# Kernel optimization log

Hardware: AMD Instinct MI355X
Metric: run time of the kernel (lower is better)

## Reference

```python
import jax, jax.numpy as jnp
import numpy as np

N_NODES = 100000
N_EDGES = 1600000
IN_CH, MID_CH, BOT_CH = 128, 128, 64


def setup_inputs() -> dict:
    key = jax.random.key(0)
    ks = jax.random.split(key, 10)
    x = jax.random.normal(ks[0], (N_NODES, IN_CH), dtype=jnp.float32)
    edge_index = jax.random.randint(ks[1], (2, N_EDGES), 0, N_NODES, dtype=jnp.int64)
    s = 0.05
    # GCNConv weights follow torch Linear convention: out = x @ W.T + b (bias added post-aggregation)
    W1 = jax.random.normal(ks[2], (MID_CH, IN_CH), dtype=jnp.float32) * s
    b1 = jnp.zeros((MID_CH,), dtype=jnp.float32)
    W2 = jax.random.normal(ks[3], (BOT_CH, MID_CH), dtype=jnp.float32) * s
    b2 = jnp.zeros((BOT_CH,), dtype=jnp.float32)
    W3 = jax.random.normal(ks[4], (MID_CH, BOT_CH), dtype=jnp.float32) * s
    b3 = jnp.zeros((MID_CH,), dtype=jnp.float32)
    W4 = jax.random.normal(ks[5], (IN_CH, MID_CH), dtype=jnp.float32) * s
    b4 = jnp.zeros((IN_CH,), dtype=jnp.float32)
    return {"x": x, "edge_index": edge_index,
            "W1": W1, "b1": b1, "W2": W2, "b2": b2,
            "W3": W3, "b3": b3, "W4": W4, "b4": b4}


def _gcn_conv(x, src, dst, norm, W, b, n):
    # linear transform first (small GEMM), then gather-normalize-scatter
    h = x @ W.T                                   # [N, out]
    msg = h[src] * norm[:, None]                  # [E+N, out] gathered messages
    out = jax.ops.segment_sum(msg, dst, num_segments=n)
    return out + b


def reference(x, edge_index, W1, b1, W2, b2, W3, b3, W4, b4):
    n = N_NODES
    # add self-loops (PyG GCNConv default)
    loop = jnp.arange(n, dtype=edge_index.dtype)
    src = jnp.concatenate([edge_index[0], loop])
    dst = jnp.concatenate([edge_index[1], loop])
    # symmetric degree normalization: deg includes self-loops -> deg >= 1
    deg = jax.ops.segment_sum(jnp.ones_like(dst, dtype=x.dtype), dst, num_segments=n)
    dinv = jax.lax.rsqrt(deg)
    norm = dinv[src] * dinv[dst]                  # [E+N]
    # encoder
    h = jax.nn.relu(_gcn_conv(x, src, dst, norm, W1, b1, n))
    z = _gcn_conv(h, src, dst, norm, W2, b2, n)
    # decoder
    h = jax.nn.relu(_gcn_conv(z, src, dst, norm, W3, b3, n))
    out = _gcn_conv(h, src, dst, norm, W4, b4, n)
    return out
```

## Files before the change

### kernel.cpp

```cpp
#include <hip/hip_runtime.h>

typedef unsigned int u32;
typedef unsigned short u16;
typedef short bf16x4 __attribute__((ext_vector_type(4)));
typedef short bf16x8 __attribute__((ext_vector_type(8)));
typedef float f32x4 __attribute__((ext_vector_type(4)));
typedef int i32x4 __attribute__((ext_vector_type(4)));
typedef long long i64x2 __attribute__((ext_vector_type(2)));

__device__ inline u16 f2bf_rne(float f) {
    u32 b = __float_as_uint(f);
    return (u16)((b + 0x7FFFu + ((b >> 16) & 1u)) >> 16);
}
__device__ inline u32 packbf2(float lo, float hi) {
    return (u32)f2bf_rne(lo) | ((u32)f2bf_rne(hi) << 16);
}
__device__ inline float bf2f(u16 h) { return __uint_as_float((u32)h << 16); }
__device__ inline float2 bfpair(u32 q) {
    float2 f;
    f.x = __uint_as_float(q << 16);
    f.y = __uint_as_float(q & 0xFFFF0000u);
    return f;
}

__global__ void k_detect(const int* __restrict__ p, int n_int32, u32* __restrict__ flag) {
    __shared__ int s[256];
    int tid = threadIdx.x;
    int acc = 0;
    int limit = n_int32 < 2048 ? n_int32 : 2048;
    for (int i = 1 + 2 * tid; i < limit; i += 512) acc |= p[i];
    s[tid] = acc;
    __syncthreads();
    for (int o = 128; o > 0; o >>= 1) {
        if (tid < o) s[tid] |= s[tid + o];
        __syncthreads();
    }
    if (tid == 0) *flag = (s[0] == 0) ? 1u : 0u;
}

template <int CIN, int COUT>
__global__ void k_wpack(const float* __restrict__ W, u16* __restrict__ Wpk) {
    int i = blockIdx.x * 256 + threadIdx.x;
    if (i >= CIN * COUT) return;
    int o = i / CIN, k = i % CIN;
    int fi = o >> 4, l15 = o & 15;
    int ks = k >> 5, w = k & 31;
    int h = w >> 4, l4 = (w & 15) >> 2, off = w & 3;
    int lane = l4 * 16 + l15;
    int e = h * 4 + off;
    constexpr int KS = CIN / 32;
    Wpk[(size_t)(((fi * KS + ks) * 64 + lane) * 8 + e)] = f2bf_rne(W[i]);
}

__global__ void k_init(u32* __restrict__ cnt, int N) {
    int i = blockIdx.x * blockDim.x + threadIdx.x;
    if (i < N) cnt[i] = 0u;
}

__global__ __launch_bounds__(256) void k_filld(const void* __restrict__ ei,
                                               const u32* __restrict__ flag,
                                               u32* __restrict__ cnt,
                                               int* __restrict__ col, int E, int N) {
    int grp = blockIdx.x & 7;
    int sub = blockIdx.x >> 3;
    int nsub = gridDim.x >> 3;
    int lo = (int)((long long)N * grp >> 3);
    int hi = (int)((long long)N * (grp + 1) >> 3);

    if (*flag) {
        const long long* p = (const long long*)ei;
        const i64x2* d2 = (const i64x2*)(p + E);
        int E2 = E >> 1;
        for (int i = sub * 256 + threadIdx.x; i < E2; i += nsub * 256) {
            i64x2 d = __builtin_nontemporal_load(d2 + i);
            int e = i << 1;
            int dx = (int)d.x, dy = (int)d.y;
            if (dx >= lo && dx < hi) {
                u32 slot = atomicAdd(&cnt[dx], 1u);
                if (slot < 64u) col[(size_t)dx * 64 + slot] =
                    (int)__builtin_nontemporal_load(p + e);
            }
            if (dy >= lo && dy < hi) {
                u32 slot = atomicAdd(&cnt[dy], 1u);
                if (slot < 64u) col[(size_t)dy * 64 + slot] =
                    (int)__builtin_nontemporal_load(p + e + 1);
            }
        }
        for (int e = (E2 << 1) + sub * 256 + threadIdx.x; e < E; e += nsub * 256) {
            int d = (int)__builtin_nontemporal_load(p + E + e);
            if (d >= lo && d < hi) {
                u32 slot = atomicAdd(&cnt[d], 1u);
                if (slot < 64u) col[(size_t)d * 64 + slot] =
                    (int)__builtin_nontemporal_load(p + e);
            }
        }
    } else {
        const int* p = (const int*)ei;
        const i32x4* d4 = (const i32x4*)(p + E);
        int E4 = E >> 2;
        for (int i = sub * 256 + threadIdx.x; i < E4; i += nsub * 256) {
            i32x4 d = __builtin_nontemporal_load(d4 + i);
            int e = i << 2;
            if (d.x >= lo && d.x < hi) {
                u32 slot = atomicAdd(&cnt[d.x], 1u);
                if (slot < 64u) col[(size_t)d.x * 64 + slot] =
                    __builtin_nontemporal_load(p + e);
            }
            if (d.y >= lo && d.y < hi) {
                u32 slot = atomicAdd(&cnt[d.y], 1u);
                if (slot < 64u) col[(size_t)d.y * 64 + slot] =
                    __builtin_nontemporal_load(p + e + 1);
            }
            if (d.z >= lo && d.z < hi) {
                u32 slot = atomicAdd(&cnt[d.z], 1u);
                if (slot < 64u) col[(size_t)d.z * 64 + slot] =
                    __builtin_nontemporal_load(p + e + 2);
            }
            if (d.w >= lo && d.w < hi) {
                u32 slot = atomicAdd(&cnt[d.w], 1u);
                if (slot < 64u) col[(size_t)d.w * 64 + slot] =
                    __builtin_nontemporal_load(p + e + 3);
            }
        }
        for (int e = (E4 << 2) + sub * 256 + threadIdx.x; e < E; e += nsub * 256) {
            int d = __builtin_nontemporal_load(p + E + e);
            if (d >= lo && d < hi) {
                u32 slot = atomicAdd(&cnt[d], 1u);
                if (slot < 64u) col[(size_t)d * 64 + slot] =
                    __builtin_nontemporal_load(p + e);
            }
        }
    }
}

__global__ void k_dinv(const u32* __restrict__ cnt, float* __restrict__ dinv, int N) {
    int i = blockIdx.x * blockDim.x + threadIdx.x;
    if (i < N) dinv[i] = rsqrtf((float)(cnt[i] + 1u));
}

template <int CIN, int COUT, int MODE, bool IN_F32>
__global__ __launch_bounds__(512, 4) void k_mgemm(const void* __restrict__ Xv,
                                                  const u16* __restrict__ Wpk,
                                                  const float* __restrict__ aux,
                                                  u16* __restrict__ Gout, int N,
                                                  int tiles, int tpb) {
    constexpr int PITCH = CIN + 8;
    constexpr int EPITCH = COUT + 8;
    constexpr int KS = CIN / 32;
    constexpr int NT = COUT / 32;
    constexpr int CHUNKS = COUT / 8;
    __shared__ __align__(16) u16 sX[64 * PITCH];
    __shared__ __align__(16) u16 sE[64 * EPITCH];

    int tid = threadIdx.x, wid = tid >> 6, lane = tid & 63;
    int l15 = lane & 15, l4 = lane >> 4;
    int rg = wid >> 1;
    int cg = wid & 1;

    bf16x8 wfrag[NT][KS];
#pragma unroll
    for (int nt = 0; nt < NT; ++nt) {
        int fi = cg * NT + nt;
#pragma unroll
        for (int ks = 0; ks < KS; ++ks)
            wfrag[nt][ks] = *(const bf16x8*)&Wpk[(size_t)(((fi * KS + ks) * 64 + lane) * 8)];
    }
    float bv[NT];
    if (MODE == 1) {
#pragma unroll
        for (int nt = 0; nt < NT; ++nt) bv[nt] = aux[cg * (COUT / 2) + nt * 16 + l15];
    }

    int t0 = blockIdx.x * tpb;
    int t1 = t0 + tpb; if (t1 > tiles) t1 = tiles;

    for (int t = t0; t < t1; ++t) {
        int rowbase = t * 64;

        if (IN_F32) {
            const float* Xf = (const float*)Xv;
            for (int i = tid * 8; i < 64 * CIN; i += 512 * 8) {
                int r = i / CIN, k = i % CIN;
                int row = rowbase + r;
                if (row >= N) row = N - 1;
                const float4* xp = (const float4*)(Xf + (size_t)row * CIN + k);
                float4 a = xp[0], b = xp[1];
                uint4 pk;
                pk.x = packbf2(a.x, a.y);
                pk.y = packbf2(a.z, a.w);
                pk.z = packbf2(b.x, b.y);
                pk.w = packbf2(b.z, b.w);
                *(uint4*)&sX[r * PITCH + k] = pk;
            }
        } else {
            const u16* Xb = (const u16*)Xv;
            for (int i = tid * 8; i < 64 * CIN; i += 512 * 8) {
                int r = i / CIN, k = i % CIN;
                int row = rowbase + r;
                if (row >= N) row = N - 1;
                *(bf16x8*)&sX[r * PITCH + k] = *(const bf16x8*)&Xb[(size_t)row * CIN + k];
            }
        }
        __syncthreads();

        f32x4 acc[NT];
#pragma unroll
        for (int nt = 0; nt < NT; ++nt) acc[nt] = (f32x4){0.f, 0.f, 0.f, 0.f};

        const u16* xrow = &sX[(rg * 16 + l15) * PITCH + 4 * l4];
#pragma unroll
        for (int ks = 0; ks < KS; ++ks) {
            bf16x4 a0 = *(const bf16x4*)(xrow + ks * 32);
            bf16x4 a1 = *(const bf16x4*)(xrow + ks * 32 + 16);
            bf16x8 av = __builtin_shufflevector(a0, a1, 0, 1, 2, 3, 4, 5, 6, 7);
#pragma unroll
            for (int nt = 0; nt < NT; ++nt)
                acc[nt] = __builtin_amdgcn_mfma_f32_16x16x32_bf16(av, wfrag[nt][ks], acc[nt], 0, 0, 0);
        }

#pragma unroll
        for (int i = 0; i < 4; ++i) {
            int rl = rg * 16 + 4 * l4 + i;
            int row = rowbase + rl;
            int rc = row < N ? row : N - 1;
            float s = (MODE == 0) ? aux[rc] : 0.f;
#pragma unroll
            for (int nt = 0; nt < NT; ++nt) {
                float a = acc[nt][i];
                float o = (MODE == 0) ? a * s : fmaxf(a + bv[nt], 0.f);
                sE[rl * EPITCH + cg * (COUT / 2) + nt * 16 + l15] = f2bf_rne(o);
            }
        }
        __syncthreads();

        for (int a = tid; a < 64 * CHUNKS; a += 512) {
            int rl = a / CHUNKS, ch = a % CHUNKS;
            int row = rowbase + rl;
            if (row < N)
                *(uint4*)&Gout[(size_t)row * COUT + ch * 8] =
                    *(const uint4*)&sE[rl * EPITCH + ch * 8];
        }
    }
}

__global__ __launch_bounds__(512, 2) void k_mgemm34(const u16* __restrict__ Xb,
                                                    const u16* __restrict__ Wp3,
                                                    const u16* __restrict__ Wp4,
                                                    const float* __restrict__ b3,
                                                    const float* __restrict__ dinv,
                                                    u16* __restrict__ Gout, int N) {
    constexpr int P1 = 72;
    constexpr int P2 = 136;
    __shared__ __align__(16) u16 sW4[128 * 128];
    __shared__ __align__(16) u16 sBuf[64 * P2];
    __shared__ __align__(16) u16 sH[64 * P2];

    int tid = threadIdx.x, wid = tid >> 6, lane = tid & 63;
    int l15 = lane & 15, l4 = lane >> 4;
    int rg = wid >> 1, cg = wid & 1;
    int rowbase = blockIdx.x * 64;

    bf16x8 wf3[4][2];
#pragma unroll
    for (int nt = 0; nt < 4; ++nt) {
        int fi = cg * 4 + nt;
#pragma unroll
        for (int ks = 0; ks < 2; ++ks)
            wf3[nt][ks] = *(const bf16x8*)&Wp3[(size_t)(((fi * 2 + ks) * 64 + lane) * 8)];
    }
    float bv[4];
#pragma unroll
    for (int nt = 0; nt < 4; ++nt) bv[nt] = b3[cg * 64 + nt * 16 + l15];

    for (int i = tid * 8; i < 128 * 128; i += 512 * 8)
        *(bf16x8*)&sW4[i] = *(const bf16x8*)&Wp4[i];

    for (int i = tid * 8; i < 64 * 64; i += 512 * 8) {
        int r = i / 64, k = i % 64;
        int row = rowbase + r;
        if (row >= N) row = N - 1;
        *(bf16x8*)&sBuf[r * P1 + k] = *(const bf16x8*)&Xb[(size_t)row * 64 + k];
    }
    __syncthreads();

    f32x4 acc[4];
#pragma unroll
    for (int nt = 0; nt < 4; ++nt) acc[nt] = (f32x4){0.f, 0.f, 0.f, 0.f};
    {
        const u16* xrow = &sBuf[(rg * 16 + l15) * P1 + 4 * l4];
#pragma unroll
        for (int ks = 0; ks < 2; ++ks) {
            bf16x4 a0 = *(const bf16x4*)(xrow + ks * 32);
            bf16x4 a1 = *(const bf16x4*)(xrow + ks * 32 + 16);
            bf16x8 av = __builtin_shufflevector(a0, a1, 0, 1, 2, 3, 4, 5, 6, 7);
#pragma unroll
            for (int nt = 0; nt < 4; ++nt)
                acc[nt] = __builtin_amdgcn_mfma_f32_16x16x32_bf16(av, wf3[nt][ks], acc[nt], 0, 0, 0);
        }
    }
#pragma unroll
    for (int i = 0; i < 4; ++i) {
        int rl = rg * 16 + 4 * l4 + i;
#pragma unroll
        for (int nt = 0; nt < 4; ++nt)
            sH[rl * P2 + cg * 64 + nt * 16 + l15] = f2bf_rne(fmaxf(acc[nt][i] + bv[nt], 0.f));
    }
    __syncthreads();

#pragma unroll
    for (int nt = 0; nt < 4; ++nt) acc[nt] = (f32x4){0.f, 0.f, 0.f, 0.f};
    {
        const u16* xrow = &sH[(rg * 16 + l15) * P2 + 4 * l4];
#pragma unroll
        for (int ks = 0; ks < 4; ++ks) {
            bf16x4 a0 = *(const bf16x4*)(xrow + ks * 32);
            bf16x4 a1 = *(const bf16x4*)(xrow + ks * 32 + 16);
            bf16x8 av = __builtin_shufflevector(a0, a1, 0, 1, 2, 3, 4, 5, 6, 7);
#pragma unroll
            for (int nt = 0; nt < 4; ++nt) {
                int fi = cg * 4 + nt;
                bf16x8 bw = *(const bf16x8*)&sW4[(size_t)(((fi * 4 + ks) * 64 + lane) * 8)];
                acc[nt] = __builtin_amdgcn_mfma_f32_16x16x32_bf16(av, bw, acc[nt], 0, 0, 0);
            }
        }
    }
#pragma unroll
    for (int i = 0; i < 4; ++i) {
        int rl = rg * 16 + 4 * l4 + i;
        int row = rowbase + rl;
        int rc = row < N ? row : N - 1;
        float s = dinv[rc];
#pragma unroll
        for (int nt = 0; nt < 4; ++nt)
            sBuf[rl * P2 + cg * 64 + nt * 16 + l15] = f2bf_rne(acc[nt][i] * s);
    }
    __syncthreads();

    for (int a = tid; a < 64 * 16; a += 512) {
        int rl = a / 16, ch = a % 16;
        int row = rowbase + rl;
        if (row < N)
            *(uint4*)&Gout[(size_t)row * 128 + ch * 8] = *(const uint4*)&sBuf[rl * P2 + ch * 8];
    }
}

template <bool OUT_BF16, bool RELU, bool HAS_BIAS>
__global__ __launch_bounds__(256) void k_spmm128(const u32* __restrict__ Gq,
                                                 const u32* __restrict__ cnt,
                                                 const int* __restrict__ col,
                                                 const float* __restrict__ dinv,
                                                 const float* __restrict__ bias,
                                                 void* __restrict__ Y, int N) {
    int wid = threadIdx.x >> 6, lane = threadIdx.x & 63;
    int v0 = blockIdx.x * 8 + wid * 2;
    if (v0 >= N) return;
    int v1 = v0 + 1;
    bool has1 = (v1 < N);

    float2 acc0 = bfpair(Gq[(size_t)v0 * 64 + lane]);
    int e0 = v0 << 6;
    int c0 = (int)cnt[v0]; if (c0 > 64) c0 = 64;
    int f0 = e0 + c0;
    float2 acc1 = {0.f, 0.f};
    int e1 = 0, f1 = 0;
    if (has1) {
        acc1 = bfpair(Gq[(size_t)v1 * 64 + lane]);
        e1 = v1 << 6;
        int c1 = (int)cnt[v1]; if (c1 > 64) c1 = 64;
        f1 = e1 + c1;
    }

    while (e0 + 8 <= f0 && e1 + 8 <= f1) {
        int u0[8], u1[8];
#pragma unroll
        for (int j = 0; j < 8; ++j) u0[j] = col[e0 + j];
#pragma unroll
        for (int j = 0; j < 8; ++j) u1[j] = col[e1 + j];
        u32 q0[8], q1[8];
#pragma unroll
        for (int j = 0; j < 8; ++j) q0[j] = Gq[(size_t)u0[j] * 64 + lane];
#pragma unroll
        for (int j = 0; j < 8; ++j) q1[j] = Gq[(size_t)u1[j] * 64 + lane];
#pragma unroll
        for (int j = 0; j < 8; ++j) {
            float2 a = bfpair(q0[j]);
            acc0.x += a.x; acc0.y += a.y;
        }
#pragma unroll
        for (int j = 0; j < 8; ++j) {
            float2 a = bfpair(q1[j]);
            acc1.x += a.x; acc1.y += a.y;
        }
        e0 += 8; e1 += 8;
    }
    for (; e0 + 8 <= f0; e0 += 8) {
        int u[8];
#pragma unroll
        for (int j = 0; j < 8; ++j) u[j] = col[e0 + j];
        u32 q[8];
#pragma unroll
        for (int j = 0; j < 8; ++j) q[j] = Gq[(size_t)u[j] * 64 + lane];
#pragma unroll
        for (int j = 0; j < 8; ++j) {
            float2 a = bfpair(q[j]);
            acc0.x += a.x; acc0.y += a.y;
        }
    }
    for (; e1 + 8 <= f1; e1 += 8) {
        int u[8];
#pragma unroll
        for (int j = 0; j < 8; ++j) u[j] = col[e1 + j];
        u32 q[8];
#pragma unroll
        for (int j = 0; j < 8; ++j) q[j] = Gq[(size_t)u[j] * 64 + lane];
#pragma unroll
        for (int j = 0; j < 8; ++j) {
            float2 a = bfpair(q[j]);
            acc1.x += a.x; acc1.y += a.y;
        }
    }
    for (; e0 < f0; ++e0) {
        float2 a = bfpair(Gq[(size_t)col[e0] * 64 + lane]);
        acc0.x += a.x; acc0.y += a.y;
    }
    for (; e1 < f1; ++e1) {
        float2 a = bfpair(Gq[(size_t)col[e1] * 64 + lane]);
        acc1.x += a.x; acc1.y += a.y;
    }

    {
        float s = dinv[v0];
        float rx = acc0.x * s, ry = acc0.y * s;
        if (HAS_BIAS) { rx += bias[2 * lane]; ry += bias[2 * lane + 1]; }
        if (RELU) { rx = fmaxf(rx, 0.f); ry = fmaxf(ry, 0.f); }
        if (OUT_BF16) ((u32*)Y)[(size_t)v0 * 64 + lane] = packbf2(rx, ry);
        else {
            float2 o2; o2.x = rx; o2.y = ry;
            *(float2*)((float*)Y + (size_t)v0 * 128 + 2 * lane) = o2;
        }
    }
    if (has1) {
        float s = dinv[v1];
        float rx = acc1.x * s, ry = acc1.y * s;
        if (HAS_BIAS) { rx += bias[2 * lane]; ry += bias[2 * lane + 1]; }
        if (RELU) { rx = fmaxf(rx, 0.f); ry = fmaxf(ry, 0.f); }
        if (OUT_BF16) ((u32*)Y)[(size_t)v1 * 64 + lane] = packbf2(rx, ry);
        else {
            float2 o2; o2.x = rx; o2.y = ry;
            *(float2*)((float*)Y + (size_t)v1 * 128 + 2 * lane) = o2;
        }
    }
}

template <bool OUT_BF16, bool RELU, bool HAS_BIAS, bool PRESCALE>
__global__ __launch_bounds__(256) void k_spmm64(const u16* __restrict__ G16,
                                                const u32* __restrict__ cnt,
                                                const int* __restrict__ col,
                                                const float* __restrict__ dinv,
                                                const float* __restrict__ bias,
                                                void* __restrict__ Y, int N) {
    int wid = threadIdx.x >> 6, lane = threadIdx.x & 63;
    int v0 = blockIdx.x * 8 + wid * 2;
    if (v0 >= N) return;
    int v1 = v0 + 1;
    bool has1 = (v1 < N);

    float acc0 = bf2f(G16[(size_t)v0 * 64 + lane]);
    int e0 = v0 << 6;
    int c0 = (int)cnt[v0]; if (c0 > 64) c0 = 64;
    int f0 = e0 + c0;
    float acc1 = 0.f;
    int e1 = 0, f1 = 0;
    if (has1) {
        acc1 = bf2f(G16[(size_t)v1 * 64 + lane]);
        e1 = v1 << 6;
        int c1 = (int)cnt[v1]; if (c1 > 64) c1 = 64;
        f1 = e1 + c1;
    }

    while (e0 + 8 <= f0 && e1 + 8 <= f1) {
        int u0[8], u1[8];
#pragma unroll
        for (int j = 0; j < 8; ++j) u0[j] = col[e0 + j];
#pragma unroll
        for (int j = 0; j < 8; ++j) u1[j] = col[e1 + j];
        u16 g0[8], g1[8];
#pragma unroll
        for (int j = 0; j < 8; ++j) g0[j] = G16[(size_t)u0[j] * 64 + lane];
#pragma unroll
        for (int j = 0; j < 8; ++j) g1[j] = G16[(size_t)u1[j] * 64 + lane];
        acc0 += ((bf2f(g0[0]) + bf2f(g0[1])) + (bf2f(g0[2]) + bf2f(g0[3]))) +
                ((bf2f(g0[4]) + bf2f(g0[5])) + (bf2f(g0[6]) + bf2f(g0[7])));
        acc1 += ((bf2f(g1[0]) + bf2f(g1[1])) + (bf2f(g1[2]) + bf2f(g1[3]))) +
                ((bf2f(g1[4]) + bf2f(g1[5])) + (bf2f(g1[6]) + bf2f(g1[7])));
        e0 += 8; e1 += 8;
    }
    for (; e0 + 8 <= f0; e0 += 8) {
        int u[8];
#pragma unroll
        for (int j = 0; j < 8; ++j) u[j] = col[e0 + j];
        u16 g[8];
#pragma unroll
        for (int j = 0; j < 8; ++j) g[j] = G16[(size_t)u[j] * 64 + lane];
        acc0 += ((bf2f(g[0]) + bf2f(g[1])) + (bf2f(g[2]) + bf2f(g[3]))) +
                ((bf2f(g[4]) + bf2f(g[5])) + (bf2f(g[6]) + bf2f(g[7])));
    }
    for (; e1 + 8 <= f1; e1 += 8) {
        int u[8];
#pragma unroll
        for (int j = 0; j < 8; ++j) u[j] = col[e1 + j];
        u16 g[8];
#pragma unroll
        for (int j = 0; j < 8; ++j) g[j] = G16[(size_t)u[j] * 64 + lane];
        acc1 += ((bf2f(g[0]) + bf2f(g[1])) + (bf2f(g[2]) + bf2f(g[3]))) +
                ((bf2f(g[4]) + bf2f(g[5])) + (bf2f(g[6]) + bf2f(g[7])));
    }
    for (; e0 < f0; ++e0) acc0 += bf2f(G16[(size_t)col[e0] * 64 + lane]);
    for (; e1 < f1; ++e1) acc1 += bf2f(G16[(size_t)col[e1] * 64 + lane]);

    {
        float s = dinv[v0];
        float r = acc0 * s;
        if (HAS_BIAS) r += bias[lane];
        if (RELU) r = fmaxf(r, 0.f);
        if (PRESCALE) r *= s;
        if (OUT_BF16) ((u16*)Y)[(size_t)v0 * 64 + lane] = f2bf_rne(r);
        else          ((float*)Y)[(size_t)v0 * 64 + lane] = r;
    }
    if (has1) {
        float s = dinv[v1];
        float r = acc1 * s;
        if (HAS_BIAS) r += bias[lane];
        if (RELU) r = fmaxf(r, 0.f);
        if (PRESCALE) r *= s;
        if (OUT_BF16) ((u16*)Y)[(size_t)v1 * 64 + lane] = f2bf_rne(r);
        else          ((float*)Y)[(size_t)v1 * 64 + lane] = r;
    }
}

extern "C" void kernel_launch(void* const* d_in, const int* in_sizes, int n_in,
                              void* d_out, int out_size, void* d_ws, size_t ws_size,
                              hipStream_t stream) {
    const float* x  = (const float*)d_in[0];
    const void*  ei = d_in[1];
    const float* W1 = (const float*)d_in[2];
    const float* b1 = (const float*)d_in[3];
    const float* W2 = (const float*)d_in[4];
    const float* b2 = (const float*)d_in[5];
    const float* W3 = (const float*)d_in[6];
    const float* b3 = (const float*)d_in[7];
    const float* W4 = (const float*)d_in[8];
    const float* b4 = (const float*)d_in[9];

    const int N = in_sizes[0] / 128;
    const int E = in_sizes[1] / 2;

    size_t off = 0;
    auto alloc = [&](size_t bytes) -> void* {
        void* p = (char*)d_ws + off;
        off += (bytes + 255) & ~(size_t)255;
        return p;
    };
    u32*   flag    = (u32*)  alloc(4);
    float* dinv    = (float*)alloc((size_t)N * 4);
    u32*   cnt     = (u32*)  alloc((size_t)N * 4);
    int*   col     = (int*)  alloc((size_t)N * 64 * 4);
    u16*   Wp1     = (u16*)  alloc(128 * 128 * 2);
    u16*   Wp2     = (u16*)  alloc(64 * 128 * 2);
    u16*   Wp3     = (u16*)  alloc(128 * 64 * 2);
    u16*   Wp4     = (u16*)  alloc(128 * 128 * 2);
    u16*   BUF1    = (u16*)  alloc((size_t)N * 128 * 2);
    u16*   BUF2    = (u16*)  alloc((size_t)N * 128 * 2);
    u16*   BUF3    = (u16*)  alloc((size_t)N * 64 * 2);
    u16*   Zbf     = (u16*)d_out;

    const int n2 = 2 * E;

    k_detect<<<1, 256, 0, stream>>>((const int*)ei, n2, flag);
    k_init<<<(N + 255) / 256, 256, 0, stream>>>(cnt, N);
    k_filld<<<4096, 256, 0, stream>>>(ei, flag, cnt, col, E, N);
    k_dinv<<<(N + 255) / 256, 256, 0, stream>>>(cnt, dinv, N);

    k_wpack<128, 128><<<(128 * 128 + 255) / 256, 256, 0, stream>>>(W1, Wp1);
    k_wpack<128, 64><<<(128 * 64 + 255) / 256, 256, 0, stream>>>(W2, Wp2);
    k_wpack<64, 128><<<(64 * 128 + 255) / 256, 256, 0, stream>>>(W3, Wp3);
    k_wpack<128, 128><<<(128 * 128 + 255) / 256, 256, 0, stream>>>(W4, Wp4);

    const int tiles = (N + 63) / 64;
    const int gM = tiles < 512 ? tiles : 512;
    const int tpb = (tiles + gM - 1) / gM;
    const int gS = (N + 7) / 8;

    k_mgemm<128, 128, 0, true><<<gM, 512, 0, stream>>>(x, Wp1, dinv, BUF1, N, tiles, tpb);
    k_spmm128<true, true, true><<<gS, 256, 0, stream>>>((const u32*)BUF1, cnt, col, dinv, b1, BUF2, N);

    k_mgemm<128, 64, 0, false><<<gM, 512, 0, stream>>>(BUF2, Wp2, dinv, BUF3, N, tiles, tpb);
    k_spmm64<true, false, true, true><<<gS, 256, 0, stream>>>(BUF3, cnt, col, dinv, b2, Zbf, N);

    k_spmm64<true, false, false, false><<<gS, 256, 0, stream>>>(Zbf, cnt, col, dinv, b2, BUF1, N);

    k_mgemm34<<<tiles, 512, 0, stream>>>(BUF1, Wp3, Wp4, b3, dinv, BUF2, N);

    k_spmm128<false, false, true><<<gS, 256, 0, stream>>>((const u32*)BUF2, cnt, col, dinv, b4, d_out, N);
}
```

Before: 405.6 us.

## Run CSR build concurrently with first GEMM in one fused launch

The adjacency fill (atomic bucket insertion) and the first layer's dense transform now share one launch: the first gM blocks do the x@W1 GEMM without dinv prescaling, and the extra blocks do the edge fill. Because dinv no longer exists when the GEMM runs, the source-side normalization moves into the first SpMM, which looks up dinv for every neighbor. This aims to overlap the latency-bound atomic fill with compute-bound GEMM work. The cost is an extra dinv gather per edge in layer one and GEMM blocks competing with atomic-heavy blocks for resources.

```diff
diff --git a/kernel.cpp b/kernel.cpp
--- a/kernel.cpp
+++ b/kernel.cpp
@@ -57,21 +57,26 @@
     if (i < N) cnt[i] = 0u;
 }
 
-__global__ __launch_bounds__(256) void k_filld(const void* __restrict__ ei,
-                                               const u32* __restrict__ flag,
-                                               u32* __restrict__ cnt,
-                                               int* __restrict__ col, int E, int N) {
-    int grp = blockIdx.x & 7;
-    int sub = blockIdx.x >> 3;
-    int nsub = gridDim.x >> 3;
+__global__ void k_dinv(const u32* __restrict__ cnt, float* __restrict__ dinv, int N) {
+    int i = blockIdx.x * blockDim.x + threadIdx.x;
+    if (i < N) dinv[i] = rsqrtf((float)(cnt[i] + 1u));
+}
+
+__device__ __forceinline__ void filld_body(const void* ei, const u32* flag,
+                                           u32* cnt, int* col, int E, int N,
+                                           int bf, int nf) {
+    int grp = bf & 7;
+    int sub = bf >> 3;
+    int nsub = nf >> 3;
     int lo = (int)((long long)N * grp >> 3);
     int hi = (int)((long long)N * (grp + 1) >> 3);
+    int tid = threadIdx.x;
 
     if (*flag) {
         const long long* p = (const long long*)ei;
         const i64x2* d2 = (const i64x2*)(p + E);
         int E2 = E >> 1;
-        for (int i = sub * 256 + threadIdx.x; i < E2; i += nsub * 256) {
+        for (int i = sub * 512 + tid; i < E2; i += nsub * 512) {
             i64x2 d = __builtin_nontemporal_load(d2 + i);
             int e = i << 1;
             int dx = (int)d.x, dy = (int)d.y;
@@ -86,7 +91,7 @@
                     (int)__builtin_nontemporal_load(p + e + 1);
             }
         }
-        for (int e = (E2 << 1) + sub * 256 + threadIdx.x; e < E; e += nsub * 256) {
+        for (int e = (E2 << 1) + sub * 512 + tid; e < E; e += nsub * 512) {
             int d = (int)__builtin_nontemporal_load(p + E + e);
             if (d >= lo && d < hi) {
                 u32 slot = atomicAdd(&cnt[d], 1u);
@@ -98,7 +103,7 @@
         const int* p = (const int*)ei;
         const i32x4* d4 = (const i32x4*)(p + E);
         int E4 = E >> 2;
-        for (int i = sub * 256 + threadIdx.x; i < E4; i += nsub * 256) {
+        for (int i = sub * 512 + tid; i < E4; i += nsub * 512) {
             i32x4 d = __builtin_nontemporal_load(d4 + i);
             int e = i << 2;
             if (d.x >= lo && d.x < hi) {
@@ -122,7 +127,7 @@
                     __builtin_nontemporal_load(p + e + 3);
             }
         }
-        for (int e = (E4 << 2) + sub * 256 + threadIdx.x; e < E; e += nsub * 256) {
+        for (int e = (E4 << 2) + sub * 512 + tid; e < E; e += nsub * 512) {
             int d = __builtin_nontemporal_load(p + E + e);
             if (d >= lo && d < hi) {
                 u32 slot = atomicAdd(&cnt[d], 1u);
@@ -133,9 +138,95 @@
     }
 }
 
-__global__ void k_dinv(const u32* __restrict__ cnt, float* __restrict__ dinv, int N) {
-    int i = blockIdx.x * blockDim.x + threadIdx.x;
-    if (i < N) dinv[i] = rsqrtf((float)(cnt[i] + 1u));
+__global__ __launch_bounds__(512, 4) void k_fused1(const float* __restrict__ Xf,
+                                                   const u16* __restrict__ Wpk,
+                                                   u16* __restrict__ Gout,
+                                                   const void* __restrict__ ei,
+                                                   const u32* __restrict__ flag,
+                                                   u32* __restrict__ cnt,
+                                                   int* __restrict__ col,
+                                                   int E, int N,
+                                                   int tiles, int tpb, int gM, int gF) {
+    constexpr int CIN = 128, COUT = 128;
+    constexpr int PITCH = CIN + 8;
+    constexpr int EPITCH = COUT + 8;
+    constexpr int KS = CIN / 32;
+    constexpr int NT = COUT / 32;
+    constexpr int CHUNKS = COUT / 8;
+    __shared__ __align__(16) u16 sX[64 * PITCH];
+    __shared__ __align__(16) u16 sE[64 * EPITCH];
+
+    if ((int)blockIdx.x >= gM) {
+        filld_body(ei, flag, cnt, col, E, N, (int)blockIdx.x - gM, gF);
+        return;
+    }
+
+    int tid = threadIdx.x, wid = tid >> 6, lane = tid & 63;
+    int l15 = lane & 15, l4 = lane >> 4;
+    int rg = wid >> 1;
+    int cg = wid & 1;
+
+    bf16x8 wfrag[NT][KS];
+#pragma unroll
+    for (int nt = 0; nt < NT; ++nt) {
+        int fi = cg * NT + nt;
+#pragma unroll
+        for (int ks = 0; ks < KS; ++ks)
+            wfrag[nt][ks] = *(const bf16x8*)&Wpk[(size_t)(((fi * KS + ks) * 64 + lane) * 8)];
+    }
+
+    int t0 = blockIdx.x * tpb;
+    int t1 = t0 + tpb; if (t1 > tiles) t1 = tiles;
+
+    for (int t = t0; t < t1; ++t) {
+        int rowbase = t * 64;
+        for (int i = tid * 8; i < 64 * CIN; i += 512 * 8) {
+            int r = i / CIN, k = i % CIN;
+            int row = rowbase + r;
+            if (row >= N) row = N - 1;
+            const float4* xp = (const float4*)(Xf + (size_t)row * CIN + k);
+            float4 a = xp[0], b = xp[1];
+            uint4 pk;
+            pk.x = packbf2(a.x, a.y);
+            pk.y = packbf2(a.z, a.w);
+            pk.z = packbf2(b.x, b.y);
+            pk.w = packbf2(b.z, b.w);
+            *(uint4*)&sX[r * PITCH + k] = pk;
+        }
+        __syncthreads();
+
+        f32x4 acc[NT];
+#pragma unroll
+        for (int nt = 0; nt < NT; ++nt) acc[nt] = (f32x4){0.f, 0.f, 0.f, 0.f};
+
+        const u16* xrow = &sX[(rg * 16 + l15) * PITCH + 4 * l4];
+#pragma unroll
+        for (int ks = 0; ks < KS; ++ks) {
+            bf16x4 a0 = *(const bf16x4*)(xrow + ks * 32);
+            bf16x4 a1 = *(const bf16x4*)(xrow + ks * 32 + 16);
+            bf16x8 av = __builtin_shufflevector(a0, a1, 0, 1, 2, 3, 4, 5, 6, 7);
+#pragma unroll
+            for (int nt = 0; nt < NT; ++nt)
+                acc[nt] = __builtin_amdgcn_mfma_f32_16x16x32_bf16(av, wfrag[nt][ks], acc[nt], 0, 0, 0);
+        }
+
+#pragma unroll
+        for (int i = 0; i < 4; ++i) {
+            int rl = rg * 16 + 4 * l4 + i;
+#pragma unroll
+            for (int nt = 0; nt < NT; ++nt)
+                sE[rl * EPITCH + cg * (COUT / 2) + nt * 16 + l15] = f2bf_rne(acc[nt][i]);
+        }
+        __syncthreads();
+
+        for (int a = tid; a < 64 * CHUNKS; a += 512) {
+            int rl = a / CHUNKS, ch = a % CHUNKS;
+            int row = rowbase + rl;
+            if (row < N)
+                *(uint4*)&Gout[(size_t)row * COUT + ch * 8] =
+                    *(const uint4*)&sE[rl * EPITCH + ch * 8];
+        }
+    }
 }
 
 template <int CIN, int COUT, int MODE, bool IN_F32>
@@ -344,7 +435,7 @@
     }
 }
 
-template <bool OUT_BF16, bool RELU, bool HAS_BIAS>
+template <bool OUT_BF16, bool RELU, bool HAS_BIAS, bool SCALE_SRC>
 __global__ __launch_bounds__(256) void k_spmm128(const u32* __restrict__ Gq,
                                                  const u32* __restrict__ cnt,
                                                  const int* __restrict__ col,
@@ -357,14 +448,19 @@
     int v1 = v0 + 1;
     bool has1 = (v1 < N);
 
+    float sv0 = dinv[v0];
     float2 acc0 = bfpair(Gq[(size_t)v0 * 64 + lane]);
+    if (SCALE_SRC) { acc0.x *= sv0; acc0.y *= sv0; }
     int e0 = v0 << 6;
     int c0 = (int)cnt[v0]; if (c0 > 64) c0 = 64;
     int f0 = e0 + c0;
+    float sv1 = 0.f;
     float2 acc1 = {0.f, 0.f};
     int e1 = 0, f1 = 0;
     if (has1) {
+        sv1 = dinv[v1];
         acc1 = bfpair(Gq[(size_t)v1 * 64 + lane]);
+        if (SCALE_SRC) { acc1.x *= sv1; acc1.y *= sv1; }
         e1 = v1 << 6;
         int c1 = (int)cnt[v1]; if (c1 > 64) c1 = 64;
         f1 = e1 + c1;
@@ -384,12 +480,14 @@
 #pragma unroll
         for (int j = 0; j < 8; ++j) {
             float2 a = bfpair(q0[j]);
-            acc0.x += a.x; acc0.y += a.y;
+            if (SCALE_SRC) { float d = dinv[u0[j]]; acc0.x += a.x * d; acc0.y += a.y * d; }
+            else           { acc0.x += a.x; acc0.y += a.y; }
         }
 #pragma unroll
         for (int j = 0; j < 8; ++j) {
             float2 a = bfpair(q1[j]);
-            acc1.x += a.x; acc1.y += a.y;
+            if (SCALE_SRC) { float d = dinv[u1[j]]; acc1.x += a.x * d; acc1.y += a.y * d; }
+            else           { acc1.x += a.x; acc1.y += a.y; }
         }
         e0 += 8; e1 += 8;
     }
@@ -403,7 +501,8 @@
 #pragma unroll
         for (int j = 0; j < 8; ++j) {
             float2 a = bfpair(q[j]);
-            acc0.x += a.x; acc0.y += a.y;
+            if (SCALE_SRC) { float d = dinv[u[j]]; acc0.x += a.x * d; acc0.y += a.y * d; }
+            else           { acc0.x += a.x; acc0.y += a.y; }
         }
     }
     for (; e1 + 8 <= f1; e1 += 8) {
@@ -416,21 +515,25 @@
 #pragma unroll
         for (int j = 0; j < 8; ++j) {
             float2 a = bfpair(q[j]);
-            acc1.x += a.x; acc1.y += a.y;
+            if (SCALE_SRC) { float d = dinv[u[j]]; acc1.x += a.x * d; acc1.y += a.y * d; }
+            else           { acc1.x += a.x; acc1.y += a.y; }
         }
     }
     for (; e0 < f0; ++e0) {
-        float2 a = bfpair(Gq[(size_t)col[e0] * 64 + lane]);
-        acc0.x += a.x; acc0.y += a.y;
+        int u = col[e0];
+        float2 a = bfpair(Gq[(size_t)u * 64 + lane]);
+        if (SCALE_SRC) { float d = dinv[u]; acc0.x += a.x * d; acc0.y += a.y * d; }
+        else           { acc0.x += a.x; acc0.y += a.y; }
     }
     for (; e1 < f1; ++e1) {
-        float2 a = bfpair(Gq[(size_t)col[e1] * 64 + lane]);
-        acc1.x += a.x; acc1.y += a.y;
+        int u = col[e1];
+        float2 a = bfpair(Gq[(size_t)u * 64 + lane]);
+        if (SCALE_SRC) { float d = dinv[u]; acc1.x += a.x * d; acc1.y += a.y * d; }
+        else           { acc1.x += a.x; acc1.y += a.y; }
     }
 
     {
-        float s = dinv[v0];
-        float rx = acc0.x * s, ry = acc0.y * s;
+        float rx = acc0.x * sv0, ry = acc0.y * sv0;
         if (HAS_BIAS) { rx += bias[2 * lane]; ry += bias[2 * lane + 1]; }
         if (RELU) { rx = fmaxf(rx, 0.f); ry = fmaxf(ry, 0.f); }
         if (OUT_BF16) ((u32*)Y)[(size_t)v0 * 64 + lane] = packbf2(rx, ry);
@@ -440,8 +543,7 @@
         }
     }
     if (has1) {
-        float s = dinv[v1];
-        float rx = acc1.x * s, ry = acc1.y * s;
+        float rx = acc1.x * sv1, ry = acc1.y * sv1;
         if (HAS_BIAS) { rx += bias[2 * lane]; ry += bias[2 * lane + 1]; }
         if (RELU) { rx = fmaxf(rx, 0.f); ry = fmaxf(ry, 0.f); }
         if (OUT_BF16) ((u32*)Y)[(size_t)v1 * 64 + lane] = packbf2(rx, ry);
@@ -575,24 +677,24 @@
     u16*   Zbf     = (u16*)d_out;
 
     const int n2 = 2 * E;
+    const int tiles = (N + 63) / 64;
+    const int gM = tiles < 512 ? tiles : 512;
+    const int tpb = (tiles + gM - 1) / gM;
+    const int gF = 2048;
+    const int gS = (N + 7) / 8;
 
     k_detect<<<1, 256, 0, stream>>>((const int*)ei, n2, flag);
     k_init<<<(N + 255) / 256, 256, 0, stream>>>(cnt, N);
-    k_filld<<<4096, 256, 0, stream>>>(ei, flag, cnt, col, E, N);
-    k_dinv<<<(N + 255) / 256, 256, 0, stream>>>(cnt, dinv, N);
-
     k_wpack<128, 128><<<(128 * 128 + 255) / 256, 256, 0, stream>>>(W1, Wp1);
     k_wpack<128, 64><<<(128 * 64 + 255) / 256, 256, 0, stream>>>(W2, Wp2);
     k_wpack<64, 128><<<(64 * 128 + 255) / 256, 256, 0, stream>>>(W3, Wp3);
     k_wpack<128, 128><<<(128 * 128 + 255) / 256, 256, 0, stream>>>(W4, Wp4);
 
-    const int tiles = (N + 63) / 64;
-    const int gM = tiles < 512 ? tiles : 512;
-    const int tpb = (tiles + gM - 1) / gM;
-    const int gS = (N + 7) / 8;
-
-    k_mgemm<128, 128, 0, true><<<gM, 512, 0, stream>>>(x, Wp1, dinv, BUF1, N, tiles, tpb);
-    k_spmm128<true, true, true><<<gS, 256, 0, stream>>>((const u32*)BUF1, cnt, col, dinv, b1, BUF2, N);
+    k_fused1<<<gM + gF, 512, 0, stream>>>(x, Wp1, BUF1, ei, flag, cnt, col,
+                                          E, N, tiles, tpb, gM, gF);
+    k_dinv<<<(N + 255) / 256, 256, 0, stream>>>(cnt, dinv, N);
+
+    k_spmm128<true, true, true, true><<<gS, 256, 0, stream>>>((const u32*)BUF1, cnt, col, dinv, b1, BUF2, N);
 
     k_mgemm<128, 64, 0, false><<<gM, 512, 0, stream>>>(BUF2, Wp2, dinv, BUF3, N, tiles, tpb);
     k_spmm64<true, false, true, true><<<gS, 256, 0, stream>>>(BUF3, cnt, col, dinv, b2, Zbf, N);
@@ -601,5 +703,5 @@
 
     k_mgemm34<<<tiles, 512, 0, stream>>>(BUF1, Wp3, Wp4, b3, dinv, BUF2, N);
 
-    k_spmm128<false, false, true><<<gS, 256, 0, stream>>>((const u32*)BUF2, cnt, col, dinv, b4, d_out, N);
-}
+    k_spmm128<false, false, true, false><<<gS, 256, 0, stream>>>((const u32*)BUF2, cnt, col, dinv, b4, d_out, N);
+}
```

After: 424.0 us. 1.05x slower.
